# Optimization experiments

Measured on AMD Instinct MI355X. Metric: run time of the kernel, lower is better.

## Reference

```python
import jax, jax.numpy as jnp
import numpy as np

B, H, L, DK = 1, 16, 2048, 64
F_FACTOR = 64            # f
MAX_SEQ = 2048           # max_seq_len
RB = MAX_SEQ // F_FACTOR # 32, out dim of f_b


def setup_inputs() -> dict:
    key = jax.random.key(0)
    ks = jax.random.split(key, 6)
    q = jax.random.normal(ks[0], (B, H, L, DK), dtype=jnp.float32)
    v = jax.random.normal(ks[1], (B, H, L, DK), dtype=jnp.float32)
    # nn.Linear weights: [out_features, in_features]
    Wa = jax.random.normal(ks[2], (F_FACTOR, DK), dtype=jnp.float32) / np.sqrt(DK)
    ba = jax.random.normal(ks[3], (F_FACTOR,), dtype=jnp.float32) * 0.02
    Wb = jax.random.normal(ks[4], (RB, DK), dtype=jnp.float32) / np.sqrt(DK)
    bb = jax.random.normal(ks[5], (RB,), dtype=jnp.float32) * 0.02
    return {"q": q, "v": v, "Wa": Wa, "ba": ba, "Wb": Wb, "bb": bb, "len_q": L}


def reference(q, v, Wa, ba, Wb, bb, len_q):
    f = Wa.shape[0]            # f
    rb = Wb.shape[0]           # max_seq_len // f
    # h_a: repeat each of the f factor channels (max_seq_len//f) times -> [B,H,L,max_seq_len], slice to len_q
    h_a = jnp.repeat(q @ Wa.T + ba, rb, axis=-1)[..., :len_q]
    # h_b: repeat each of the (max_seq_len//f) channels f times
    h_b = jnp.repeat(q @ Wb.T + bb, f, axis=-1)[..., :len_q]
    # dense_attn = h_a @ h_b^T  -> [B,H,L,L]
    dense_attn = jnp.einsum('bhik,bhjk->bhij', h_a, h_b)
    # mask=None path; dropout inactive (eval / p=0)
    dense_attn = jax.nn.softmax(dense_attn, axis=-1)
    output = jnp.matmul(dense_attn, v)  # [B,H,L,DK]
    return (output, dense_attn)
```

## Files before the change

kernel.cpp:

```cpp
#include <hip/hip_runtime.h>
#include <hip/hip_bf16.h>


#define HN 16
#define LN 2048
#define KR 32

typedef __attribute__((ext_vector_type(8))) short bf16x8;
typedef __attribute__((ext_vector_type(4))) float f32x4;

__device__ __forceinline__ float b2f(unsigned short u) {
    return __uint_as_float(((unsigned int)u) << 16);
}
__device__ __forceinline__ unsigned short f2b(float f) {
    __hip_bfloat16 h = __float2bfloat16(f);
    return *reinterpret_cast<unsigned short*>(&h);
}
__device__ __forceinline__ void glds16(const void* g, void* l) {
    __builtin_amdgcn_global_load_lds(
        (const __attribute__((address_space(1))) unsigned int*)g,
        (__attribute__((address_space(3))) unsigned int*)l, 16, 0, 0);
}

#define TILE_B 4096
#define TILE_V 4096

__global__ __launch_bounds__(256) void k_cb(
    const float* __restrict__ q,
    const float* __restrict__ Wa, const float* __restrict__ ba,
    const float* __restrict__ Wb, const float* __restrict__ bb,
    unsigned short* __restrict__ Chi, unsigned short* __restrict__ Clo,
    unsigned short* __restrict__ TileB)
{
    __shared__ float sWa[64 * 64];
    __shared__ float sWb[32 * 64];
    __shared__ float sba[64];
    __shared__ float sbb[32];
    const int tid = threadIdx.x;
    for (int i = tid; i < 64 * 64; i += 256) sWa[i] = Wa[i];
    for (int i = tid; i < 32 * 64; i += 256) sWb[i] = Wb[i];
    if (tid < 64) sba[tid] = ba[tid];
    if (tid < 32) sbb[tid] = bb[tid];
    __syncthreads();

    const int t = blockIdx.x * 256 + tid;
    const int row = t >> 2, kg = t & 3, mh = kg * 8;
    const int h = row >> 11, i = row & 2047;
    const int jc = i >> 6, c = i & 63;

    float qf[64];
    const float4* q4p = reinterpret_cast<const float4*>(q + (size_t)row * 64);
    #pragma unroll
    for (int k4 = 0; k4 < 16; ++k4) {
        float4 u = q4p[k4];
        qf[4*k4+0] = u.x; qf[4*k4+1] = u.y; qf[4*k4+2] = u.z; qf[4*k4+3] = u.w;
    }
    unsigned short chb[8], clb[8], bhb[8], blb[8];
    #pragma unroll
    for (int mi = 0; mi < 8; ++mi) {
        const int m = mh + mi;
        float a0 = sba[2*m], a1 = sba[2*m+1], bv = sbb[m];
        const float4* wa0 = reinterpret_cast<const float4*>(&sWa[(2*m) * 64]);
        const float4* wa1 = reinterpret_cast<const float4*>(&sWa[(2*m+1) * 64]);
        const float4* wb0 = reinterpret_cast<const float4*>(&sWb[m * 64]);
        #pragma unroll
        for (int k4 = 0; k4 < 16; ++k4) {
            float4 w0 = wa0[k4], w1 = wa1[k4], w2 = wb0[k4];
            float x0 = qf[4*k4], x1 = qf[4*k4+1], x2 = qf[4*k4+2], x3 = qf[4*k4+3];
            a0 = fmaf(x0, w0.x, a0); a0 = fmaf(x1, w0.y, a0);
            a0 = fmaf(x2, w0.z, a0); a0 = fmaf(x3, w0.w, a0);
            a1 = fmaf(x0, w1.x, a1); a1 = fmaf(x1, w1.y, a1);
            a1 = fmaf(x2, w1.z, a1); a1 = fmaf(x3, w1.w, a1);
            bv = fmaf(x0, w2.x, bv); bv = fmaf(x1, w2.y, bv);
            bv = fmaf(x2, w2.z, bv); bv = fmaf(x3, w2.w, bv);
        }
        float cc = 32.f * (a0 + a1);
        unsigned short ch = f2b(cc);
        chb[mi] = ch; clb[mi] = f2b(cc - b2f(ch));
        unsigned short bh = f2b(bv);
        bhb[mi] = bh; blb[mi] = f2b(bv - b2f(bh));
    }
    *reinterpret_cast<uint4*>(Chi + (size_t)row * KR + mh) = *reinterpret_cast<uint4*>(chb);
    *reinterpret_cast<uint4*>(Clo + (size_t)row * KR + mh) = *reinterpret_cast<uint4*>(clb);
    unsigned short* tb = TileB + (size_t)(h * 32 + jc) * TILE_B + (kg * 64 + c) * 8;
    *reinterpret_cast<uint4*>(tb)        = *reinterpret_cast<uint4*>(bhb);
    *reinterpret_cast<uint4*>(tb + 2048) = *reinterpret_cast<uint4*>(blb);
}

__global__ __launch_bounds__(256) void k_vtc(
    const float* __restrict__ v, unsigned short* __restrict__ TileV)
{
    __shared__ unsigned short sv[64 * 66];
    const int tid = threadIdx.x;
    const int h = blockIdx.x >> 5, jc = blockIdx.x & 31;
    const float* src = v + (size_t)(h * LN + jc * 64) * 64;
    for (int i = tid; i < 4096; i += 256)
        sv[(i >> 6) * 66 + (i & 63)] = f2b(src[i]);
    __syncthreads();
    unsigned short* vt = TileV + (size_t)(h * 32 + jc) * TILE_V;
    #pragma unroll
    for (int it = 0; it < 2; ++it) {
        const int gi = tid + it * 256;
        const int jg = gi >> 6, d = gi & 63;
        unsigned short g8[8];
        #pragma unroll
        for (int jj = 0; jj < 8; ++jj)
            g8[jj] = sv[(jg * 8 + jj) * 66 + d];
        *reinterpret_cast<uint4*>(vt + (jg * 64 + d) * 8) = *reinterpret_cast<uint4*>(g8);
    }
}

__global__ __launch_bounds__(256, 2) void k_fuse(
    const unsigned short* __restrict__ Chi, const unsigned short* __restrict__ Clo,
    const unsigned short* __restrict__ TileB, const unsigned short* __restrict__ TileV,
    float* __restrict__ outO, float* __restrict__ outP)
{
    __shared__ unsigned short sB[2][TILE_B];
    __shared__ unsigned short sV[2][TILE_V];
    __shared__ unsigned short ps[2][16 * 72];
    __shared__ float sRedM[4][16];
    __shared__ float sRedL[4][16];

    const int b = blockIdx.x;
    const int h = (b & 7) * 2 + (b >> 10);
    const int tile = (b >> 3) & 127;
    const int tid = threadIdx.x, w = tid >> 6, lane = tid & 63;
    const int quad = lane >> 4, n16 = lane & 15;
    const int rbase = tile * 16;
    const int hL = h * LN;

    const bf16x8 ahi = *reinterpret_cast<const bf16x8*>(Chi + (size_t)(hL + rbase + n16) * KR + quad * 8);
    const bf16x8 alo = *reinterpret_cast<const bf16x8*>(Clo + (size_t)(hL + rbase + n16) * KR + quad * 8);

    const char* bBase = (const char*)(TileB + (size_t)(h * 32) * TILE_B);
    const char* vBase = (const char*)(TileV + (size_t)(h * 32) * TILE_V);
    const int srcOff = w * 2048 + lane * 16;
    const int fragW = (quad * 64 + w * 16 + n16) * 8;

    f32x4 zero = {0.f, 0.f, 0.f, 0.f};
    f32x4 sS[32];

    {
        char* d = (char*)sB[0];
        glds16(bBase + srcOff,        d + w * 2048);
        glds16(bBase + srcOff + 1024, d + w * 2048 + 1024);
    }
    #pragma unroll
    for (int jc = 0; jc < 32; ++jc) {
        const int cur = jc & 1;
        __syncthreads();
        if (jc + 1 < 32) {
            const char* g = bBase + (size_t)(jc + 1) * (TILE_B * 2);
            char* d = (char*)sB[cur ^ 1];
            glds16(g + srcOff,        d + w * 2048);
            glds16(g + srcOff + 1024, d + w * 2048 + 1024);
        }
        const unsigned short* t = sB[cur];
        bf16x8 bhi = *reinterpret_cast<const bf16x8*>(t + fragW);
        bf16x8 blo = *reinterpret_cast<const bf16x8*>(t + 2048 + fragW);
        f32x4 acc = zero;
        acc = __builtin_amdgcn_mfma_f32_16x16x32_bf16(ahi, bhi, acc, 0, 0, 0);
        acc = __builtin_amdgcn_mfma_f32_16x16x32_bf16(ahi, blo, acc, 0, 0, 0);
        acc = __builtin_amdgcn_mfma_f32_16x16x32_bf16(alo, bhi, acc, 0, 0, 0);
        sS[jc] = acc;
    }

    float mr[4], li[4];
    {
        float m0[4];
        #pragma unroll
        for (int r = 0; r < 4; ++r) {
            float mm = sS[0][r];
            #pragma unroll
            for (int jc = 1; jc < 32; ++jc) mm = fmaxf(mm, sS[jc][r]);
            #pragma unroll
            for (int off = 1; off <= 8; off <<= 1)
                mm = fmaxf(mm, __shfl_xor(mm, off, 64));
            m0[r] = mm;
        }
        __syncthreads();
        if (n16 == 0) {
            #pragma unroll
            for (int r = 0; r < 4; ++r) sRedM[w][quad * 4 + r] = m0[r];
        }
        __syncthreads();
        #pragma unroll
        for (int r = 0; r < 4; ++r)
            mr[r] = fmaxf(fmaxf(sRedM[0][quad*4+r], sRedM[1][quad*4+r]),
                          fmaxf(sRedM[2][quad*4+r], sRedM[3][quad*4+r]));
        float l0[4] = {0.f, 0.f, 0.f, 0.f};
        #pragma unroll
        for (int jc = 0; jc < 32; ++jc) {
            #pragma unroll
            for (int r = 0; r < 4; ++r) {
                float p = __expf(sS[jc][r] - mr[r]);
                sS[jc][r] = p;
                l0[r] += p;
            }
        }
        #pragma unroll
        for (int r = 0; r < 4; ++r) {
            float ll = l0[r];
            #pragma unroll
            for (int off = 1; off <= 8; off <<= 1)
                ll += __shfl_xor(ll, off, 64);
            l0[r] = ll;
        }
        if (n16 == 0) {
            #pragma unroll
            for (int r = 0; r < 4; ++r) sRedL[w][quad * 4 + r] = l0[r];
        }
        __syncthreads();
        #pragma unroll
        for (int r = 0; r < 4; ++r)
            li[r] = 1.f / (sRedL[0][quad*4+r] + sRedL[1][quad*4+r]
                         + sRedL[2][quad*4+r] + sRedL[3][quad*4+r]);
    }

    f32x4 o = zero;
    {
        char* d = (char*)sV[0];
        glds16(vBase + srcOff,        d + w * 2048);
        glds16(vBase + srcOff + 1024, d + w * 2048 + 1024);
        #pragma unroll
        for (int r = 0; r < 4; ++r)
            ps[0][(quad * 4 + r) * 72 + w * 16 + n16] = f2b(sS[0][r]);
    }
    #pragma unroll
    for (int jc = 0; jc < 32; ++jc) {
        const int cur = jc & 1;
        __syncthreads();
        if (jc + 1 < 32) {
            const char* g = vBase + (size_t)(jc + 1) * (TILE_V * 2);
            char* d = (char*)sV[cur ^ 1];
            glds16(g + srcOff,        d + w * 2048);
            glds16(g + srcOff + 1024, d + w * 2048 + 1024);
            #pragma unroll
            for (int r = 0; r < 4; ++r)
                ps[cur ^ 1][(quad * 4 + r) * 72 + w * 16 + n16] = f2b(sS[jc + 1][r]);
        }
        const int jb = jc * 64;
        #pragma unroll
        for (int r = 0; r < 4; ++r)
            __builtin_nontemporal_store(sS[jc][r] * li[r],
                outP + (size_t)(hL + rbase + quad * 4 + r) * LN + jb + w * 16 + n16);
        #pragma unroll
        for (int ks = 0; ks < 2; ++ks) {
            bf16x8 pa = *reinterpret_cast<const bf16x8*>(&ps[cur][n16 * 72 + ks * 32 + quad * 8]);
            bf16x8 vb = *reinterpret_cast<const bf16x8*>(
                sV[cur] + ((ks * 4 + quad) * 64 + w * 16 + n16) * 8);
            o = __builtin_amdgcn_mfma_f32_16x16x32_bf16(pa, vb, o, 0, 0, 0);
        }
    }
    #pragma unroll
    for (int r = 0; r < 4; ++r)
        __builtin_nontemporal_store(o[r] * li[r],
            &outO[(size_t)(hL + rbase + quad * 4 + r) * 64 + w * 16 + n16]);
}

extern "C" void kernel_launch(void* const* d_in, const int* in_sizes, int n_in,
                              void* d_out, int out_size, void* d_ws, size_t ws_size,
                              hipStream_t stream)
{
    (void)in_sizes; (void)n_in; (void)out_size; (void)ws_size;
    const float* q  = (const float*)d_in[0];
    const float* v  = (const float*)d_in[1];
    const float* Wa = (const float*)d_in[2];
    const float* ba = (const float*)d_in[3];
    const float* Wb = (const float*)d_in[4];
    const float* bb = (const float*)d_in[5];

    float* out = (float*)d_out;
    char* wsb = (char*)d_ws;
    const size_t MB = 1024 * 1024;
    unsigned short* Chi   = (unsigned short*)(wsb);
    unsigned short* Clo   = (unsigned short*)(wsb + 2 * MB);
    unsigned short* TileB = (unsigned short*)(wsb + 4 * MB);
    unsigned short* TileV = (unsigned short*)(wsb + 8 * MB);

    float* outO = out;
    float* outP = out + (size_t)HN * LN * 64;

    hipLaunchKernelGGL(k_cb, dim3(512), dim3(256), 0, stream,
                       q, Wa, ba, Wb, bb, Chi, Clo, TileB);
    hipLaunchKernelGGL(k_vtc, dim3(512), dim3(256), 0, stream, v, TileV);
    hipLaunchKernelGGL(k_fuse, dim3(2048), dim3(256), 0, stream,
                       Chi, Clo, TileB, TileV, outO, outP);
}
```

Before: 412.0 us.

## Load B and V tiles directly from global memory instead of staging in LDS

The fused attention kernel no longer double-buffers B and V tiles through shared memory with global_load_lds. Each wave now reads its MFMA fragments straight from global or L2, which removes the per-chunk __syncthreads barriers. The probability tile is written to LDS in two halves of 16 chunks, so only two barriers remain in the PV phase. The trade is that data reuse and prefetch overlap from LDS staging are lost, with more reliance on L2 and cache hits for tiles shared by blocks of the same head.

```diff
diff --git a/kernel.cpp b/kernel.cpp
--- a/kernel.cpp
+++ b/kernel.cpp
@@ -15,11 +15,6 @@
 __device__ __forceinline__ unsigned short f2b(float f) {
     __hip_bfloat16 h = __float2bfloat16(f);
     return *reinterpret_cast<unsigned short*>(&h);
-}
-__device__ __forceinline__ void glds16(const void* g, void* l) {
-    __builtin_amdgcn_global_load_lds(
-        (const __attribute__((address_space(1))) unsigned int*)g,
-        (__attribute__((address_space(3))) unsigned int*)l, 16, 0, 0);
 }
 
 #define TILE_B 4096
@@ -110,14 +105,13 @@
     }
 }
 
+#define PS_STRIDE 1032
 __global__ __launch_bounds__(256, 2) void k_fuse(
     const unsigned short* __restrict__ Chi, const unsigned short* __restrict__ Clo,
     const unsigned short* __restrict__ TileB, const unsigned short* __restrict__ TileV,
     float* __restrict__ outO, float* __restrict__ outP)
 {
-    __shared__ unsigned short sB[2][TILE_B];
-    __shared__ unsigned short sV[2][TILE_V];
-    __shared__ unsigned short ps[2][16 * 72];
+    __shared__ unsigned short ps[16 * PS_STRIDE];
     __shared__ float sRedM[4][16];
     __shared__ float sRedL[4][16];
 
@@ -132,32 +126,18 @@
     const bf16x8 ahi = *reinterpret_cast<const bf16x8*>(Chi + (size_t)(hL + rbase + n16) * KR + quad * 8);
     const bf16x8 alo = *reinterpret_cast<const bf16x8*>(Clo + (size_t)(hL + rbase + n16) * KR + quad * 8);
 
-    const char* bBase = (const char*)(TileB + (size_t)(h * 32) * TILE_B);
-    const char* vBase = (const char*)(TileV + (size_t)(h * 32) * TILE_V);
-    const int srcOff = w * 2048 + lane * 16;
+    const unsigned short* bTile = TileB + (size_t)(h * 32) * TILE_B;
+    const unsigned short* vTile = TileV + (size_t)(h * 32) * TILE_V;
     const int fragW = (quad * 64 + w * 16 + n16) * 8;
 
     f32x4 zero = {0.f, 0.f, 0.f, 0.f};
     f32x4 sS[32];
 
-    {
-        char* d = (char*)sB[0];
-        glds16(bBase + srcOff,        d + w * 2048);
-        glds16(bBase + srcOff + 1024, d + w * 2048 + 1024);
-    }
     #pragma unroll
     for (int jc = 0; jc < 32; ++jc) {
-        const int cur = jc & 1;
-        __syncthreads();
-        if (jc + 1 < 32) {
-            const char* g = bBase + (size_t)(jc + 1) * (TILE_B * 2);
-            char* d = (char*)sB[cur ^ 1];
-            glds16(g + srcOff,        d + w * 2048);
-            glds16(g + srcOff + 1024, d + w * 2048 + 1024);
-        }
-        const unsigned short* t = sB[cur];
-        bf16x8 bhi = *reinterpret_cast<const bf16x8*>(t + fragW);
-        bf16x8 blo = *reinterpret_cast<const bf16x8*>(t + 2048 + fragW);
+        const unsigned short* g = bTile + jc * TILE_B;
+        bf16x8 bhi = *reinterpret_cast<const bf16x8*>(g + fragW);
+        bf16x8 blo = *reinterpret_cast<const bf16x8*>(g + 2048 + fragW);
         f32x4 acc = zero;
         acc = __builtin_amdgcn_mfma_f32_16x16x32_bf16(ahi, bhi, acc, 0, 0, 0);
         acc = __builtin_amdgcn_mfma_f32_16x16x32_bf16(ahi, blo, acc, 0, 0, 0);
@@ -178,7 +158,6 @@
                 mm = fmaxf(mm, __shfl_xor(mm, off, 64));
             m0[r] = mm;
         }
-        __syncthreads();
         if (n16 == 0) {
             #pragma unroll
             for (int r = 0; r < 4; ++r) sRedM[w][quad * 4 + r] = m0[r];
@@ -218,38 +197,35 @@
     }
 
     f32x4 o = zero;
-    {
-        char* d = (char*)sV[0];
-        glds16(vBase + srcOff,        d + w * 2048);
-        glds16(vBase + srcOff + 1024, d + w * 2048 + 1024);
-        #pragma unroll
-        for (int r = 0; r < 4; ++r)
-            ps[0][(quad * 4 + r) * 72 + w * 16 + n16] = f2b(sS[0][r]);
-    }
-    #pragma unroll
-    for (int jc = 0; jc < 32; ++jc) {
-        const int cur = jc & 1;
+    #pragma unroll
+    for (int half = 0; half < 2; ++half) {
+        if (half) __syncthreads();
+        const int jc0 = half * 16;
+        #pragma unroll
+        for (int ji = 0; ji < 16; ++ji) {
+            #pragma unroll
+            for (int r = 0; r < 4; ++r)
+                ps[(quad * 4 + r) * PS_STRIDE + ji * 64 + w * 16 + n16]
+                    = f2b(sS[jc0 + ji][r]);
+        }
         __syncthreads();
-        if (jc + 1 < 32) {
-            const char* g = vBase + (size_t)(jc + 1) * (TILE_V * 2);
-            char* d = (char*)sV[cur ^ 1];
-            glds16(g + srcOff,        d + w * 2048);
-            glds16(g + srcOff + 1024, d + w * 2048 + 1024);
+        #pragma unroll
+        for (int ji = 0; ji < 16; ++ji) {
+            const int jc = jc0 + ji;
+            const int jb = jc * 64;
             #pragma unroll
             for (int r = 0; r < 4; ++r)
-                ps[cur ^ 1][(quad * 4 + r) * 72 + w * 16 + n16] = f2b(sS[jc + 1][r]);
-        }
-        const int jb = jc * 64;
-        #pragma unroll
-        for (int r = 0; r < 4; ++r)
-            __builtin_nontemporal_store(sS[jc][r] * li[r],
-                outP + (size_t)(hL + rbase + quad * 4 + r) * LN + jb + w * 16 + n16);
-        #pragma unroll
-        for (int ks = 0; ks < 2; ++ks) {
-            bf16x8 pa = *reinterpret_cast<const bf16x8*>(&ps[cur][n16 * 72 + ks * 32 + quad * 8]);
-            bf16x8 vb = *reinterpret_cast<const bf16x8*>(
-                sV[cur] + ((ks * 4 + quad) * 64 + w * 16 + n16) * 8);
-            o = __builtin_amdgcn_mfma_f32_16x16x32_bf16(pa, vb, o, 0, 0, 0);
+                __builtin_nontemporal_store(sS[jc][r] * li[r],
+                    outP + (size_t)(hL + rbase + quad * 4 + r) * LN + jb + w * 16 + n16);
+            const unsigned short* vt = vTile + jc * TILE_V;
+            #pragma unroll
+            for (int ks = 0; ks < 2; ++ks) {
+                bf16x8 pa = *reinterpret_cast<const bf16x8*>(
+                    ps + n16 * PS_STRIDE + ji * 64 + ks * 32 + quad * 8);
+                bf16x8 vb = *reinterpret_cast<const bf16x8*>(
+                    vt + ((ks * 4 + quad) * 64 + w * 16 + n16) * 8);
+                o = __builtin_amdgcn_mfma_f32_16x16x32_bf16(pa, vb, o, 0, 0, 0);
+            }
         }
     }
     #pragma unroll
```

After: 384.3 us. 1.07x faster.
